# Kernel optimization log

Measured on AMD Instinct MI355X. Metric: run time of the kernel, lower is better.

Reference implementation:

```python
import jax, jax.numpy as jnp
import numpy as np

B, T, C, L = 1024, 256, 128, 64
NEG = -1e30  # finite stand-in for -inf (safe gradients)
EPS = 1e-7   # keras.backend.epsilon()


def setup_inputs() -> dict:
    key = jax.random.key(0)
    k1, k2 = jax.random.split(key)
    # y_pred is a softmax output (probabilities), as keras ctc_batch_cost expects
    logits = jax.random.normal(k1, (B, T, C), dtype=jnp.float32)
    y_pred = jax.nn.softmax(logits, axis=-1)
    # labels in [0, C-2]; class C-1 is the CTC blank (keras convention)
    y_true = jax.random.randint(k2, (B, L), 0, C - 1, dtype=jnp.int64)
    return {"y_true": y_true, "y_pred": y_pred}


def ctc_loss(y_true, y_pred):
    """Negative log-likelihood CTC loss per sample, shape [B, 1].
    Matches keras.backend.ctc_batch_cost with full input/label lengths,
    blank index = num_classes - 1, log(y_pred + eps)."""
    Bb, Tt, Cc = y_pred.shape
    Ll = y_true.shape[1]
    blank = Cc - 1
    S = 2 * Ll + 1  # extended label: blank, l1, blank, l2, ..., blank

    logp = jnp.log(y_pred + EPS)  # [B, T, C]

    ext = jnp.full((Bb, S), blank, dtype=y_true.dtype).at[:, 1::2].set(y_true)  # [B, S]
    # per-(t, s) log-prob of the extended symbol: lp[b, t, s] = logp[b, t, ext[b, s]]
    lp = jnp.take_along_axis(logp, ext[:, None, :], axis=2)  # [B, T, S]

    # skip transition s-2 -> s allowed iff ext[s] != blank and ext[s] != ext[s-2]
    ext_m2 = jnp.concatenate(
        [jnp.full((Bb, 2), blank, dtype=ext.dtype), ext[:, :-2]], axis=1)
    can_skip = (ext != blank) & (ext != ext_m2)  # [B, S]

    def shift1(a):
        return jnp.concatenate(
            [jnp.full((Bb, 1), NEG, dtype=a.dtype), a[:, :-1]], axis=1)

    # alpha init at t=0: only s=0 (blank) and s=1 (first label) reachable
    alpha0 = (jnp.full((Bb, S), NEG, dtype=lp.dtype)
              .at[:, 0].set(lp[:, 0, 0])
              .at[:, 1].set(lp[:, 0, 1]))

    def step(alpha, lp_t):
        a1 = shift1(alpha)
        a2 = jnp.where(can_skip, shift1(shift1(alpha)), NEG)
        new = jax.nn.logsumexp(jnp.stack([alpha, a1, a2], axis=0), axis=0) + lp_t
        return new, None

    lp_tbs = jnp.swapaxes(lp, 0, 1)  # [T, B, S]
    alpha, _ = jax.lax.scan(step, alpha0, lp_tbs[1:])

    log_lik = jnp.logaddexp(alpha[:, S - 1], alpha[:, S - 2])  # end on last blank or last label
    return -log_lik[:, None]  # [B, 1], matching ctc_batch_cost output shape


def reference(y_true, y_pred):
    return ctc_loss(y_true, y_pred)
```

## Files before the change

kernel.cpp:

```cpp
#include <hip/hip_runtime.h>
#include <math.h>


#define Bn 1024
#define Tn 256
#define Cn 128
#define Ln 64
#define BLANK 127
#define NEG2 (-1.0e30f)
#define EPSV (1e-7f)
#define U 8
#define NG (Tn / U)

#if __has_builtin(__builtin_amdgcn_exp2f)
#define EXP2(x) __builtin_amdgcn_exp2f(x)
#else
#define EXP2(x) exp2f(x)
#endif
#if __has_builtin(__builtin_amdgcn_logf)
#define LOG2(x) __builtin_amdgcn_logf(x)
#else
#define LOG2(x) log2f(x)
#endif

__global__ __launch_bounds__(64)
void ctc_wave_kernel(const int* __restrict__ y_true,
                     const float* __restrict__ y_pred,
                     float* __restrict__ out) {
    const int b = blockIdx.x;
    const int i = threadIdx.x;

    const int* lab = y_true + b * Ln;
    const int  li   = lab[i];
    const int  lim1 = (i == 0) ? -1 : lab[i - 1];
    const bool skip = (li != lim1);

    const float* base   = y_pred + (size_t)b * (Tn * Cn);
    const float* pl_ptr = base + li;
    const float* pb_ptr = base + BLANK;

    const int baddr = ((i - 1) & 63) << 2;

    float lpl[2][U], lpb[2][U];
    {
        float rl[U], rb[U];
        #pragma unroll
        for (int j = 0; j < U; ++j) {
            rl[j] = pl_ptr[j * Cn];
            rb[j] = pb_ptr[j * Cn];
        }
        #pragma unroll
        for (int j = 0; j < U; ++j) {
            lpl[0][j] = LOG2(rl[j] + EPSV);
            lpb[0][j] = LOG2(rb[j] + EPSV);
        }
    }

    float A0 = NEG2, Aod = NEG2, Aev = NEG2;

    for (int g = 0; g < NG; ++g) {
        const int cur = g & 1, nxt = cur ^ 1;
        float rl[U], rb[U];
        if (g + 1 < NG) {
            const float* pl2 = pl_ptr + (size_t)(g + 1) * U * Cn;
            const float* pb2 = pb_ptr + (size_t)(g + 1) * U * Cn;
            #pragma unroll
            for (int j = 0; j < U; ++j) {
                rl[j] = pl2[j * Cn];
                rb[j] = pb2[j * Cn];
            }
        }
        #pragma unroll
        for (int j = 0; j < U; ++j) {
            const float lb = lpb[cur][j];
            const float ll = lpl[cur][j];
            if (g == 0 && j == 0) {
                A0  = lb;
                Aod = (i == 0) ? ll : NEG2;
                Aev = NEG2;
                continue;
            }
            const float odL_raw = __int_as_float(
                __builtin_amdgcn_ds_bpermute(baddr, __float_as_int(Aod)));
            const float evL_raw = __int_as_float(
                __builtin_amdgcn_ds_bpermute(baddr, __float_as_int(Aev)));
            const float evL = (i == 0) ? A0   : evL_raw;
            const float odL = (i == 0) ? NEG2 : odL_raw;

            const float m2  = fmaxf(Aev, Aod);
            const float d2  = fminf(Aev, Aod) - m2;
            const float nev = m2 + LOG2(1.0f + EXP2(d2)) + lb;

            const float c3  = skip ? odL : NEG2;
            const float m3  = fmaxf(fmaxf(Aod, evL), c3);
            const float s3  = EXP2(Aod - m3) + EXP2(evL - m3) + EXP2(c3 - m3);
            const float nod = m3 + LOG2(s3) + ll;

            A0 += lb;
            Aod = nod;
            Aev = nev;
        }
        if (g + 1 < NG) {
            #pragma unroll
            for (int j = 0; j < U; ++j) {
                lpl[nxt][j] = LOG2(rl[j] + EPSV);
                lpb[nxt][j] = LOG2(rb[j] + EPSV);
            }
        }
    }

    if (i == 63) {
        const float m = fmaxf(Aev, Aod);
        const float d = fminf(Aev, Aod) - m;
        const float ll2 = m + LOG2(1.0f + EXP2(d));
        out[b] = -(ll2 * 0.69314718055994530942f);
    }
}

extern "C" void kernel_launch(void* const* d_in, const int* in_sizes, int n_in,
                              void* d_out, int out_size, void* d_ws, size_t ws_size,
                              hipStream_t stream) {
    const int*   y_true = (const int*)d_in[0];
    const float* y_pred = (const float*)d_in[1];
    float*       out    = (float*)d_out;
    hipLaunchKernelGGL(ctc_wave_kernel, dim3(Bn), dim3(64), 0, stream,
                       y_true, y_pred, out);
}
```

Before: 197.6 us.

## Run CTC recursion in scaled probability space with DPP shifts and per-group renormalization

Replaces the log-space logsumexp recursion with a linear-probability forward pass. Inputs are scaled by 128 and the wave-wide maximum is renormalized every 8 steps, with the exponent tracked as an integer, so the transcendental exp/log calls in the inner loop go away. Lane shifts and the max reduction use DPP moves instead of ds_bpermute, and loads are double-buffered two groups ahead. The risk is underflow or precision loss within a group, since scaling is only applied every 8 steps.

```diff
diff --git a/kernel.cpp b/kernel.cpp
--- a/kernel.cpp
+++ b/kernel.cpp
@@ -7,113 +7,115 @@
 #define Cn 128
 #define Ln 64
 #define BLANK 127
-#define NEG2 (-1.0e30f)
-#define EPSV (1e-7f)
 #define U 8
 #define NG (Tn / U)
+#define EPS128 (1e-7f * 128.0f)
+#define LN2 0.69314718055994530942f
 
-#if __has_builtin(__builtin_amdgcn_exp2f)
-#define EXP2(x) __builtin_amdgcn_exp2f(x)
-#else
-#define EXP2(x) exp2f(x)
-#endif
-#if __has_builtin(__builtin_amdgcn_logf)
-#define LOG2(x) __builtin_amdgcn_logf(x)
-#else
-#define LOG2(x) log2f(x)
-#endif
+template <int CTRL>
+__device__ __forceinline__ float dpp_mov(float x) {
+    return __int_as_float(__builtin_amdgcn_update_dpp(
+        0, __float_as_int(x), CTRL, 0xF, 0xF, true));
+}
 
 __global__ __launch_bounds__(64)
-void ctc_wave_kernel(const int* __restrict__ y_true,
+void ctc_prob_kernel(const int* __restrict__ y_true,
                      const float* __restrict__ y_pred,
                      float* __restrict__ out) {
     const int b = blockIdx.x;
     const int i = threadIdx.x;
+    const bool lane0 = (i == 0);
 
     const int* lab = y_true + b * Ln;
-    const int  li   = lab[i];
-    const int  lim1 = (i == 0) ? -1 : lab[i - 1];
-    const bool skip = (li != lim1);
+    const int li   = lab[i];
+    const int prev = lab[(i == 0) ? 0 : (i - 1)];
+    const bool skip = (i == 0) || (li != prev);
 
-    const float* base   = y_pred + (size_t)b * (Tn * Cn);
-    const float* pl_ptr = base + li;
-    const float* pb_ptr = base + BLANK;
+    const float* base = y_pred + (size_t)b * (Tn * Cn);
+    const float* pl = base + li;
+    const float* pb = base + BLANK;
 
-    const int baddr = ((i - 1) & 63) << 2;
+    float rlA[U], rbA[U], rlB[U], rbB[U], ql[U], qb[U];
+    float A0 = 0.0f, Aod = 0.0f, Aev = 0.0f;
+    int Esum = 0;
 
-    float lpl[2][U], lpb[2][U];
-    {
-        float rl[U], rb[U];
-        #pragma unroll
+    auto issue = [&](int g, float* rl, float* rb) {
+        const float* l  = pl + (size_t)g * (U * Cn);
+        const float* bl = pb + (size_t)g * (U * Cn);
+#pragma unroll
+        for (int j = 0; j < U; ++j) { rl[j] = l[j * Cn]; rb[j] = bl[j * Cn]; }
+    };
+    auto convert = [&](const float* rl, const float* rb) {
+#pragma unroll
         for (int j = 0; j < U; ++j) {
-            rl[j] = pl_ptr[j * Cn];
-            rb[j] = pb_ptr[j * Cn];
+            ql[j] = fmaf(rl[j], 128.0f, EPS128);
+            qb[j] = fmaf(rb[j], 128.0f, EPS128);
         }
-        #pragma unroll
+    };
+    auto steps = [&](bool first) {
+#pragma unroll
         for (int j = 0; j < U; ++j) {
-            lpl[0][j] = LOG2(rl[j] + EPSV);
-            lpb[0][j] = LOG2(rb[j] + EPSV);
-        }
-    }
-
-    float A0 = NEG2, Aod = NEG2, Aev = NEG2;
-
-    for (int g = 0; g < NG; ++g) {
-        const int cur = g & 1, nxt = cur ^ 1;
-        float rl[U], rb[U];
-        if (g + 1 < NG) {
-            const float* pl2 = pl_ptr + (size_t)(g + 1) * U * Cn;
-            const float* pb2 = pb_ptr + (size_t)(g + 1) * U * Cn;
-            #pragma unroll
-            for (int j = 0; j < U; ++j) {
-                rl[j] = pl2[j * Cn];
-                rb[j] = pb2[j * Cn];
-            }
-        }
-        #pragma unroll
-        for (int j = 0; j < U; ++j) {
-            const float lb = lpb[cur][j];
-            const float ll = lpl[cur][j];
-            if (g == 0 && j == 0) {
-                A0  = lb;
-                Aod = (i == 0) ? ll : NEG2;
-                Aev = NEG2;
+            if (first && j == 0) {
+                A0  = qb[0];
+                Aod = lane0 ? ql[0] : 0.0f;
+                Aev = 0.0f;
                 continue;
             }
-            const float odL_raw = __int_as_float(
-                __builtin_amdgcn_ds_bpermute(baddr, __float_as_int(Aod)));
-            const float evL_raw = __int_as_float(
-                __builtin_amdgcn_ds_bpermute(baddr, __float_as_int(Aev)));
-            const float evL = (i == 0) ? A0   : evL_raw;
-            const float odL = (i == 0) ? NEG2 : odL_raw;
-
-            const float m2  = fmaxf(Aev, Aod);
-            const float d2  = fminf(Aev, Aod) - m2;
-            const float nev = m2 + LOG2(1.0f + EXP2(d2)) + lb;
-
-            const float c3  = skip ? odL : NEG2;
-            const float m3  = fmaxf(fmaxf(Aod, evL), c3);
-            const float s3  = EXP2(Aod - m3) + EXP2(evL - m3) + EXP2(c3 - m3);
-            const float nod = m3 + LOG2(s3) + ll;
-
-            A0 += lb;
+            const float odL = dpp_mov<0x138>(Aod);
+            const float evS = dpp_mov<0x138>(Aev);
+            const float evL = lane0 ? A0 : evS;
+            const float sk  = skip ? odL : 0.0f;
+            const float nev = (Aev + Aod) * qb[j];
+            const float nod = (Aod + evL + sk) * ql[j];
+            A0 *= qb[j];
             Aod = nod;
             Aev = nev;
         }
-        if (g + 1 < NG) {
-            #pragma unroll
-            for (int j = 0; j < U; ++j) {
-                lpl[nxt][j] = LOG2(rl[j] + EPSV);
-                lpb[nxt][j] = LOG2(rb[j] + EPSV);
-            }
-        }
+    };
+    auto renorm = [&]() {
+        float m = fmaxf(A0, fmaxf(Aod, Aev));
+        m = fmaxf(m, dpp_mov<0x111>(m));
+        m = fmaxf(m, dpp_mov<0x112>(m));
+        m = fmaxf(m, dpp_mov<0x114>(m));
+        m = fmaxf(m, dpp_mov<0x118>(m));
+        m = fmaxf(m, dpp_mov<0x142>(m));
+        m = fmaxf(m, dpp_mov<0x143>(m));
+        const unsigned ub = (unsigned)__builtin_amdgcn_readlane(__float_as_int(m), 63);
+        const int ebits = (int)(ub >> 23);
+        const float sc = __int_as_float((254 - ebits) << 23);
+        Esum += ebits - 127;
+        A0 *= sc; Aod *= sc; Aev *= sc;
+    };
+
+    issue(0, rlA, rbA);
+    issue(1, rlB, rbB);
+    convert(rlA, rbA);
+    issue(2, rlA, rbA);
+    steps(true);
+    renorm();
+
+    for (int g = 1; g < NG - 1; g += 2) {
+        convert(rlB, rbB);
+        if (g + 2 < NG) issue(g + 2, rlB, rbB);
+        steps(false);
+        renorm();
+        convert(rlA, rbA);
+        if (g + 3 < NG) issue(g + 3, rlA, rbA);
+        steps(false);
+        renorm();
     }
 
+    convert(rlB, rbB);
+    steps(false);
+
     if (i == 63) {
-        const float m = fmaxf(Aev, Aod);
-        const float d = fminf(Aev, Aod) - m;
-        const float ll2 = m + LOG2(1.0f + EXP2(d));
-        out[b] = -(ll2 * 0.69314718055994530942f);
+        const float s  = Aod + Aev;
+#if __has_builtin(__builtin_amdgcn_logf)
+        const float l2 = __builtin_amdgcn_logf(s) + (float)(Esum - 7 * Tn);
+#else
+        const float l2 = log2f(s) + (float)(Esum - 7 * Tn);
+#endif
+        out[b] = -l2 * LN2;
     }
 }
 
@@ -123,6 +125,6 @@
     const int*   y_true = (const int*)d_in[0];
     const float* y_pred = (const float*)d_in[1];
     float*       out    = (float*)d_out;
-    hipLaunchKernelGGL(ctc_wave_kernel, dim3(Bn), dim3(64), 0, stream,
+    hipLaunchKernelGGL(ctc_prob_kernel, dim3(Bn), dim3(64), 0, stream,
                        y_true, y_pred, out);
 }
```

Result: no change. 193.8 us (-1.9%).
